# Performance work log

Hardware: AMD Instinct MI355X
Metric: run time of the kernel (lower is better)

The kernel has to match this reference:

```python
import jax, jax.numpy as jnp
import numpy as np

N, DEG, FIN, HID, OUT = 50000, 16, 128, 128, 64


def setup_inputs() -> dict:
    key = jax.random.key(0)
    ks = jax.random.split(key, 32)
    x = jax.random.normal(ks[0], (N, FIN), dtype=jnp.float32)
    src = jax.random.randint(ks[1], (N * DEG,), 0, N, dtype=jnp.int32)
    dst = jnp.repeat(jnp.arange(N, dtype=jnp.int32), DEG)  # sorted by target, fixed degree
    edge_index = jnp.stack([src, dst])  # [2, E]
    dims = [(FIN, HID), (HID, HID), (HID, OUT)]
    params = {}
    i = 2
    for l, (fi, fo) in enumerate(dims, 1):
        s_lstm = 1.0 / np.sqrt(fi)
        params[f"W_ih{l}"] = jax.random.normal(ks[i + 0], (4 * fi, fi)) * s_lstm
        params[f"W_hh{l}"] = jax.random.normal(ks[i + 1], (4 * fi, fi)) * s_lstm
        params[f"b_ih{l}"] = jax.random.normal(ks[i + 2], (4 * fi,)) * s_lstm
        params[f"b_hh{l}"] = jax.random.normal(ks[i + 3], (4 * fi,)) * s_lstm
        params[f"Wl{l}"] = jax.random.normal(ks[i + 4], (fo, fi)) * (1.0 / np.sqrt(fi))
        params[f"bl{l}"] = jnp.zeros((fo,), jnp.float32)
        params[f"Wr{l}"] = jax.random.normal(ks[i + 5], (fo, fi)) * (1.0 / np.sqrt(fi))
        i += 6
    return {"x": x, "edge_index": edge_index, **params}


def _lstm_last(neigh, Wih, Whh, bih, bhh):
    # neigh: [N, deg, Fi]; PyTorch LSTM gate order i,f,g,o; return last-step output h.
    h0 = jnp.zeros((neigh.shape[0], Wih.shape[0] // 4), neigh.dtype)
    bias = bih + bhh

    def step(carry, xt):
        h, c = carry
        g = xt @ Wih.T + h @ Whh.T + bias
        i, f, gg, o = jnp.split(g, 4, axis=-1)
        c = jax.nn.sigmoid(f) * c + jax.nn.sigmoid(i) * jnp.tanh(gg)
        h = jax.nn.sigmoid(o) * jnp.tanh(c)
        return (h, c), None

    (h, _), _ = jax.lax.scan(step, (h0, h0), jnp.swapaxes(neigh, 0, 1))
    return h


def _sage_layer(x, src2d, Wih, Whh, bih, bhh, Wl, bl, Wr):
    neigh = x[src2d]  # gather: [N, deg, Fi]
    aggr = _lstm_last(neigh, Wih, Whh, bih, bhh)  # [N, Fi]
    return aggr @ Wl.T + bl + x @ Wr.T  # lin_l(aggr) + lin_r(x)


def reference(x, edge_index,
              W_ih1, W_hh1, b_ih1, b_hh1, Wl1, bl1, Wr1,
              W_ih2, W_hh2, b_ih2, b_hh2, Wl2, bl2, Wr2,
              W_ih3, W_hh3, b_ih3, b_hh3, Wl3, bl3, Wr3):
    n = x.shape[0]
    src2d = edge_index[0].reshape(n, -1)  # fixed-degree, dst-sorted edge list
    h = _sage_layer(x, src2d, W_ih1, W_hh1, b_ih1, b_hh1, Wl1, bl1, Wr1)
    h = jax.nn.relu(h)  # dropout is identity in eval mode
    h = _sage_layer(h, src2d, W_ih2, W_hh2, b_ih2, b_hh2, Wl2, bl2, Wr2)
    h = jax.nn.relu(h)
    return _sage_layer(h, src2d, W_ih3, W_hh3, b_ih3, b_hh3, Wl3, bl3, Wr3)
```

## Files before the change

### kernel.cpp

```cpp
#include <hip/hip_runtime.h>
#include <cstddef>
#include <cstdint>

typedef __attribute__((ext_vector_type(4))) float f32x4;
typedef __attribute__((ext_vector_type(8))) short short8;

#define HID 128
#define NK1 -1.4426950408889634f
#define PK2 2.8853900817779268f

#define BAR_LGKM() __asm__ volatile("s_waitcnt lgkmcnt(0)\ns_barrier" ::: "memory")
#define STEP_BAR() __asm__ volatile("s_waitcnt vmcnt(0) lgkmcnt(0)\ns_barrier" ::: "memory")

__device__ __forceinline__ short f2bf(float f) {
  unsigned u = __builtin_bit_cast(unsigned, f);
  u += 0x7FFFu + ((u >> 16) & 1u);
  return (short)(u >> 16);
}
__device__ __forceinline__ unsigned pack_bf2(float a, float b) {
  unsigned ua = __builtin_bit_cast(unsigned, a) + 0x8000u;
  unsigned ub = __builtin_bit_cast(unsigned, b) + 0x8000u;
  return __builtin_amdgcn_perm(ub, ua, 0x07060302u);
}
__device__ __forceinline__ float2 unpack2v(int w) {
  float2 r;
  r.x = __builtin_bit_cast(float, (unsigned)(w << 16));
  r.y = __builtin_bit_cast(float, (unsigned)w & 0xffff0000u);
  return r;
}

__device__ __forceinline__ float lstm_elem(float si, float sf, float sg, float so, float& c) {
  float Ei = __builtin_amdgcn_exp2f(si);
  float Ef = __builtin_amdgcn_exp2f(sf);
  float Tg = __builtin_amdgcn_exp2f(sg);
  float Eo = __builtin_amdgcn_exp2f(so);
  float u = 1.0f + Ei, w = 1.0f + Ef, v = Tg + 1.0f, Tm = Tg - 1.0f;
  float t0 = u * v;
  float num = __builtin_fmaf(c, t0, w * Tm);
  float cn = num * __builtin_amdgcn_rcpf(w * t0);
  c = cn;
  float Tc = __builtin_amdgcn_exp2f(PK2 * cn);
  return (Tc - 1.0f) * __builtin_amdgcn_rcpf((1.0f + Eo) * (Tc + 1.0f));
}

__global__ void conv_x_kernel(const float* __restrict__ x, short* __restrict__ xb, int n) {
  int i = blockIdx.x * blockDim.x + threadIdx.x;
  int stride = gridDim.x * blockDim.x;
  for (; i < n; i += stride) xb[i] = f2bf(x[i]);
}

__global__ void conv_layer_kernel(const float* __restrict__ Wih, const float* __restrict__ Whh,
                                  const float* __restrict__ bih, const float* __restrict__ bhh,
                                  const float* __restrict__ Wl, const float* __restrict__ Wr, int foK,
                                  short* __restrict__ wihB, short* __restrict__ whhB,
                                  short* __restrict__ wlB, short* __restrict__ wrB,
                                  float* __restrict__ bsum) {
  int i = blockIdx.x * blockDim.x + threadIdx.x;
  if (i < 512 * HID) {
    float sc = ((i >> 14) == 2) ? PK2 : NK1;
    wihB[i] = f2bf(Wih[i] * sc);
    whhB[i] = f2bf(Whh[i] * sc);
  }
  if (i < foK) { wlB[i] = f2bf(Wl[i]); wrB[i] = f2bf(Wr[i]); }
  if (i < 512) bsum[i] = (bih[i] + bhh[i]) * (((i >> 7) == 2) ? PK2 : NK1);
}

#define OSTR 524
__global__ __launch_bounds__(512, 4) void pgemm_kernel(
    const short* __restrict__ A, const short* __restrict__ W,
    const float* __restrict__ bias, short* __restrict__ out, int M, int ntiles) {
  __shared__ short ldsO[32 * OSTR];
  const int tid = threadIdx.x;
  const int wave = tid >> 6, lane = tid & 63;
  const int quad = lane >> 4, nn = lane & 15;
  const int cbase = wave * 64;

  short8 wreg[4][4];
#pragma unroll
  for (int kt = 0; kt < 4; ++kt)
#pragma unroll
    for (int nt = 0; nt < 4; ++nt)
      wreg[kt][nt] = *(const short8*)(W + (size_t)(cbase + nt * 16 + nn) * HID + kt * 32 + quad * 8);
  f32x4 bias4[4];
#pragma unroll
  for (int nt = 0; nt < 4; ++nt)
#pragma unroll
    for (int r = 0; r < 4; ++r) bias4[nt][r] = bias[cbase + nt * 16 + quad * 4 + r];

#pragma unroll 1
  for (int rt = blockIdx.x; rt < ntiles; rt += gridDim.x) {
    const int row0 = rt * 32;
    f32x4 acc[2][4];
#pragma unroll
    for (int b = 0; b < 2; ++b)
#pragma unroll
      for (int nt = 0; nt < 4; ++nt) acc[b][nt] = bias4[nt];
#pragma unroll
    for (int kt = 0; kt < 4; ++kt) {
      int r0 = row0 + nn;      if (r0 > M - 1) r0 = M - 1;
      int r1 = row0 + 16 + nn; if (r1 > M - 1) r1 = M - 1;
      short8 af0 = *(const short8*)(A + (size_t)r0 * HID + kt * 32 + quad * 8);
      short8 af1 = *(const short8*)(A + (size_t)r1 * HID + kt * 32 + quad * 8);
#pragma unroll
      for (int nt = 0; nt < 4; ++nt) {
        acc[0][nt] = __builtin_amdgcn_mfma_f32_16x16x32_bf16(wreg[kt][nt], af0, acc[0][nt], 0, 0, 0);
        acc[1][nt] = __builtin_amdgcn_mfma_f32_16x16x32_bf16(wreg[kt][nt], af1, acc[1][nt], 0, 0, 0);
      }
    }
    BAR_LGKM();
#pragma unroll
    for (int b = 0; b < 2; ++b)
#pragma unroll
      for (int nt = 0; nt < 4; ++nt) {
        uint2 pk;
        pk.x = pack_bf2(acc[b][nt][0], acc[b][nt][1]);
        pk.y = pack_bf2(acc[b][nt][2], acc[b][nt][3]);
        *(uint2*)(ldsO + (b * 16 + nn) * OSTR + cbase + nt * 16 + quad * 4) = pk;
      }
    BAR_LGKM();
#pragma unroll
    for (int idx = tid; idx < 32 * 64; idx += 512) {
      int row = idx >> 6, c8 = (idx & 63) * 8;
      if (row0 + row < M)
        *(short8*)(out + (size_t)(row0 + row) * 512 + c8) = *(const short8*)(ldsO + row * OSTR + c8);
    }
  }
}

template <int FO, bool RELU, bool OUTF32>
__global__ __launch_bounds__(256, 4) void outgemm_kernel(
    const short* __restrict__ A1, const short* __restrict__ W1,
    const short* __restrict__ A2, const short* __restrict__ W2,
    const float* __restrict__ bias,
    short* __restrict__ outB, float* __restrict__ outF, int M, int ntiles) {
  const int NTW = FO / 64;
  __shared__ char osm[8704];
  short* ldsO = (short*)osm;
  float* ldsF = (float*)osm;
  const int tid = threadIdx.x;
  const int wave = tid >> 6, lane = tid & 63;
  const int quad = lane >> 4, nn = lane & 15;
  const int cbase = wave * (FO / 4);

  short8 w1r[4][NTW], w2r[4][NTW];
#pragma unroll
  for (int kt = 0; kt < 4; ++kt)
#pragma unroll
    for (int nt = 0; nt < NTW; ++nt) {
      w1r[kt][nt] = *(const short8*)(W1 + (size_t)(cbase + nt * 16 + nn) * HID + kt * 32 + quad * 8);
      w2r[kt][nt] = *(const short8*)(W2 + (size_t)(cbase + nt * 16 + nn) * HID + kt * 32 + quad * 8);
    }
  f32x4 bias4[NTW];
#pragma unroll
  for (int nt = 0; nt < NTW; ++nt)
#pragma unroll
    for (int r = 0; r < 4; ++r) bias4[nt][r] = bias[cbase + nt * 16 + quad * 4 + r];

#pragma unroll 1
  for (int rt = blockIdx.x; rt < ntiles; rt += gridDim.x) {
    const int row0 = rt * 32;
    f32x4 acc[2][NTW];
#pragma unroll
    for (int b = 0; b < 2; ++b)
#pragma unroll
      for (int nt = 0; nt < NTW; ++nt) acc[b][nt] = bias4[nt];

#pragma unroll
    for (int kt = 0; kt < 4; ++kt) {
      int r0 = row0 + nn;      if (r0 > M - 1) r0 = M - 1;
      int r1 = row0 + 16 + nn; if (r1 > M - 1) r1 = M - 1;
      short8 a10 = *(const short8*)(A1 + (size_t)r0 * HID + kt * 32 + quad * 8);
      short8 a11 = *(const short8*)(A1 + (size_t)r1 * HID + kt * 32 + quad * 8);
      short8 a20 = *(const short8*)(A2 + (size_t)r0 * HID + kt * 32 + quad * 8);
      short8 a21 = *(const short8*)(A2 + (size_t)r1 * HID + kt * 32 + quad * 8);
#pragma unroll
      for (int nt = 0; nt < NTW; ++nt) {
        acc[0][nt] = __builtin_amdgcn_mfma_f32_16x16x32_bf16(w1r[kt][nt], a10, acc[0][nt], 0, 0, 0);
        acc[1][nt] = __builtin_amdgcn_mfma_f32_16x16x32_bf16(w1r[kt][nt], a11, acc[1][nt], 0, 0, 0);
        acc[0][nt] = __builtin_amdgcn_mfma_f32_16x16x32_bf16(w2r[kt][nt], a20, acc[0][nt], 0, 0, 0);
        acc[1][nt] = __builtin_amdgcn_mfma_f32_16x16x32_bf16(w2r[kt][nt], a21, acc[1][nt], 0, 0, 0);
      }
    }
    BAR_LGKM();
#pragma unroll
    for (int b = 0; b < 2; ++b)
#pragma unroll
      for (int nt = 0; nt < NTW; ++nt) {
        f32x4 v = acc[b][nt];
        if (RELU) {
#pragma unroll
          for (int r = 0; r < 4; ++r) v[r] = fmaxf(v[r], 0.0f);
        }
        int lrow = b * 16 + nn;
        if (OUTF32) {
          *(f32x4*)(ldsF + lrow * 68 + cbase + nt * 16 + quad * 4) = v;
        } else {
          uint2 pk;
          pk.x = pack_bf2(v[0], v[1]);
          pk.y = pack_bf2(v[2], v[3]);
          *(uint2*)(ldsO + lrow * 136 + cbase + nt * 16 + quad * 4) = pk;
        }
      }
    BAR_LGKM();
    if (OUTF32) {
#pragma unroll
      for (int idx = tid; idx < 32 * 16; idx += 256) {
        int row = idx >> 4, c4 = (idx & 15) * 4;
        if (row0 + row < M)
          *(f32x4*)(outF + (size_t)(row0 + row) * 64 + c4) = *(const f32x4*)(ldsF + row * 68 + c4);
      }
    } else {
#pragma unroll
      for (int idx = tid; idx < 32 * 16; idx += 256) {
        int row = idx >> 4, c8 = (idx & 15) * 8;
        if (row0 + row < M)
          *(short8*)(outB + (size_t)(row0 + row) * 128 + c8) = *(const short8*)(ldsO + row * 136 + c8);
      }
    }
  }
}

#define NPB 16
#define PSTR 520
#define HSTR 152
#define LSTM_LDS_BYTES ((2 * NPB * PSTR + 2 * NPB * HSTR) * 2 + 256 * 4)

__global__ __launch_bounds__(512, 4) void lstm_steps_kernel(
    const short* __restrict__ P, const short* __restrict__ Whh,
    const int* __restrict__ src, short* __restrict__ aggr, int M, int ntiles) {
  extern __shared__ char smem[];
  short* Pb = (short*)smem;
  short* Hb = Pb + 2 * NPB * PSTR;
  int* srcL = (int*)(Hb + 2 * NPB * HSTR);

  const int tid = threadIdx.x;
  const int wave = tid >> 6, lane = tid & 63;
  const int quad = lane >> 4, nn = lane & 15;
  const int r0row = wave * 2, r1row = wave * 2 + 1;

  short8 wreg[4][4];
#pragma unroll
  for (int kt = 0; kt < 4; ++kt)
#pragma unroll
    for (int q = 0; q < 4; ++q)
      wreg[kt][q] = *(const short8*)(Whh + (size_t)(q * 128 + wave * 16 + nn) * HID + kt * 32 + quad * 8);

#pragma unroll 1
  for (int tile = blockIdx.x; tile < ntiles; tile += gridDim.x) {
    const int nodeBase = tile * NPB;
    if (tid < 256) {
      int node = nodeBase + (tid >> 4);
      srcL[tid] = (node < M) ? src[nodeBase * 16 + tid] : 0;
    }
    float c_st[4] = {0.f, 0.f, 0.f, 0.f};
    BAR_LGKM();

    int sA = srcL[r0row * 16 + 0], sB = srcL[r1row * 16 + 0];
    __builtin_amdgcn_global_load_lds(
        (const __attribute__((address_space(1))) unsigned int*)(P + (size_t)sA * 512 + lane * 8),
        (__attribute__((address_space(3))) unsigned int*)(Pb + r0row * PSTR), 16, 0, 0);
    __builtin_amdgcn_global_load_lds(
        (const __attribute__((address_space(1))) unsigned int*)(P + (size_t)sB * 512 + lane * 8),
        (__attribute__((address_space(3))) unsigned int*)(Pb + r1row * PSTR), 16, 0, 0);
    sA = srcL[r0row * 16 + 1];
    sB = srcL[r1row * 16 + 1];

#pragma unroll 1
    for (int t = 0; t < 16; ++t) {
      short* Pc = Pb + (t & 1) * NPB * PSTR;
      short* Pn = Pb + ((t + 1) & 1) * NPB * PSTR;
      const short* Hp = Hb + ((t + 1) & 1) * NPB * HSTR;
      short* Hw = Hb + (t & 1) * NPB * HSTR;

      STEP_BAR();

      const short* pR = Pc + nn * PSTR + wave * 16 + quad * 4;
      uint2 p0 = *(const uint2*)(pR + 0 * 128);
      uint2 p1 = *(const uint2*)(pR + 1 * 128);
      uint2 p2 = *(const uint2*)(pR + 2 * 128);
      uint2 p3 = *(const uint2*)(pR + 3 * 128);
      f32x4 acc[4];
      {
        float2 a0 = unpack2v(p0.x), a1 = unpack2v(p0.y);
        acc[0][0] = a0.x; acc[0][1] = a0.y; acc[0][2] = a1.x; acc[0][3] = a1.y;
        float2 b0 = unpack2v(p1.x), b1 = unpack2v(p1.y);
        acc[1][0] = b0.x; acc[1][1] = b0.y; acc[1][2] = b1.x; acc[1][3] = b1.y;
        float2 c0 = unpack2v(p2.x), c1 = unpack2v(p2.y);
        acc[2][0] = c0.x; acc[2][1] = c0.y; acc[2][2] = c1.x; acc[2][3] = c1.y;
        float2 d0 = unpack2v(p3.x), d1 = unpack2v(p3.y);
        acc[3][0] = d0.x; acc[3][1] = d0.y; acc[3][2] = d1.x; acc[3][3] = d1.y;
      }

      if (t < 15) {
        __builtin_amdgcn_global_load_lds(
            (const __attribute__((address_space(1))) unsigned int*)(P + (size_t)sA * 512 + lane * 8),
            (__attribute__((address_space(3))) unsigned int*)(Pn + r0row * PSTR), 16, 0, 0);
        __builtin_amdgcn_global_load_lds(
            (const __attribute__((address_space(1))) unsigned int*)(P + (size_t)sB * 512 + lane * 8),
            (__attribute__((address_space(3))) unsigned int*)(Pn + r1row * PSTR), 16, 0, 0);
        int tn = (t + 2 < 16) ? t + 2 : 15;
        sA = srcL[r0row * 16 + tn];
        sB = srcL[r1row * 16 + tn];
      }

      if (t) {
#pragma unroll
        for (int kt = 0; kt < 4; ++kt) {
          short8 hb = *(const short8*)(Hp + nn * HSTR + kt * 32 + quad * 8);
#pragma unroll
          for (int q = 0; q < 4; ++q)
            acc[q] = __builtin_amdgcn_mfma_f32_16x16x32_bf16(wreg[kt][q], hb, acc[q], 0, 0, 0);
        }
      }

      float hv[4];
#pragma unroll
      for (int r = 0; r < 4; ++r)
        hv[r] = lstm_elem(acc[0][r], acc[1][r], acc[2][r], acc[3][r], c_st[r]);
      uint2 pk;
      pk.x = pack_bf2(hv[0], hv[1]);
      pk.y = pack_bf2(hv[2], hv[3]);
      *(uint2*)(Hw + nn * HSTR + wave * 16 + quad * 4) = pk;
    }

    BAR_LGKM();
    if (tid < 256) {
      int rrow = tid >> 4, off = (tid & 15) * 8;
      int node = nodeBase + rrow;
      if (node < M)
        *(short8*)(aggr + (size_t)node * HID + off) = *(const short8*)(Hb + NPB * HSTR + rrow * HSTR + off);
    }
  }
}

extern "C" void kernel_launch(void* const* d_in, const int* in_sizes, int n_in,
                              void* d_out, int out_size, void* d_ws, size_t ws_size,
                              hipStream_t stream) {
  const float* x = (const float*)d_in[0];
  const int* src = (const int*)d_in[1];
  const float* Wih[3] = {(const float*)d_in[2], (const float*)d_in[9], (const float*)d_in[16]};
  const float* Whh[3] = {(const float*)d_in[3], (const float*)d_in[10], (const float*)d_in[17]};
  const float* bih[3] = {(const float*)d_in[4], (const float*)d_in[11], (const float*)d_in[18]};
  const float* bhh[3] = {(const float*)d_in[5], (const float*)d_in[12], (const float*)d_in[19]};
  const float* Wl[3]  = {(const float*)d_in[6], (const float*)d_in[13], (const float*)d_in[20]};
  const float* bl[3]  = {(const float*)d_in[7], (const float*)d_in[14], (const float*)d_in[21]};
  const float* Wr[3]  = {(const float*)d_in[8], (const float*)d_in[15], (const float*)d_in[22]};

  const int M = in_sizes[0] / HID;

  char* ws = (char*)d_ws;
  size_t off = 0;
  auto alloc = [&](size_t bytes) -> void* {
    void* p = ws + off;
    off += (bytes + 255) & ~(size_t)255;
    return p;
  };
  short* curA = (short*)alloc((size_t)M * HID * 2);
  short* curB = (short*)alloc((size_t)M * HID * 2);
  short* aggr = (short*)alloc((size_t)M * HID * 2);
  short* Pbuf = (short*)alloc((size_t)M * 512 * 2);
  short* wihB[3]; short* whhB[3]; short* wlB[3]; short* wrB[3]; float* bsum[3];
  for (int l = 0; l < 3; ++l) {
    wihB[l] = (short*)alloc(512 * HID * 2);
    whhB[l] = (short*)alloc(512 * HID * 2);
    wlB[l]  = (short*)alloc(HID * HID * 2);
    wrB[l]  = (short*)alloc(HID * HID * 2);
    bsum[l] = (float*)alloc(512 * 4);
  }

  const int nltiles = (M + NPB - 1) / NPB;
  const int ntiles = (M + 31) / 32;

  (void)hipFuncSetAttribute((const void*)lstm_steps_kernel,
                            hipFuncAttributeMaxDynamicSharedMemorySize, LSTM_LDS_BYTES);

  conv_x_kernel<<<2048, 256, 0, stream>>>(x, curA, M * HID);
  for (int l = 0; l < 3; ++l) {
    const int Fo = (l == 2) ? 64 : 128;
    conv_layer_kernel<<<256, 256, 0, stream>>>(Wih[l], Whh[l], bih[l], bhh[l], Wl[l], Wr[l],
                                               Fo * HID, wihB[l], whhB[l], wlB[l], wrB[l], bsum[l]);
  }

  short* cur = curA;
  short* nxt = curB;
  for (int l = 0; l < 3; ++l) {
    pgemm_kernel<<<784, 512, 0, stream>>>(cur, wihB[l], bsum[l], Pbuf, M, ntiles);
    lstm_steps_kernel<<<768, 512, LSTM_LDS_BYTES, stream>>>(Pbuf, whhB[l], src, aggr, M, nltiles);
    if (l < 2) {
      outgemm_kernel<128, true, false><<<784, 256, 0, stream>>>(
          aggr, wlB[l], cur, wrB[l], bl[l], nxt, nullptr, M, ntiles);
      short* tswap = cur; cur = nxt; nxt = tswap;
    } else {
      outgemm_kernel<64, false, true><<<784, 256, 0, stream>>>(
          aggr, wlB[l], cur, wrB[l], bl[l], nullptr, (float*)d_out, M, ntiles);
    }
  }
}
```

Baseline: 811.9 us.

## Triple-buffer gathered P rows in LSTM step kernel with two-step prefetch

The LSTM recurrence kernel now keeps three LDS buffers for the gathered input-projection rows instead of two, and issues loads two timesteps ahead. The per-step barrier waits with vmcnt(2) instead of vmcnt(0), so one step's gather can stay in flight while the current step computes. This hides more random-gather latency behind the serial MFMA/gate work, at the cost of more LDS per block (possibly lower occupancy). Grid size drops from 768 to 512 blocks. Loads are now issued every step, including redundant ones at the tail.

```diff
diff --git a/kernel.cpp b/kernel.cpp
--- a/kernel.cpp
+++ b/kernel.cpp
@@ -10,7 +10,7 @@
 #define PK2 2.8853900817779268f
 
 #define BAR_LGKM() __asm__ volatile("s_waitcnt lgkmcnt(0)\ns_barrier" ::: "memory")
-#define STEP_BAR() __asm__ volatile("s_waitcnt vmcnt(0) lgkmcnt(0)\ns_barrier" ::: "memory")
+#define STEP_BAR2() __asm__ volatile("s_waitcnt vmcnt(2) lgkmcnt(0)\ns_barrier" ::: "memory")
 
 __device__ __forceinline__ short f2bf(float f) {
   unsigned u = __builtin_bit_cast(unsigned, f);
@@ -223,14 +223,14 @@
 #define NPB 16
 #define PSTR 520
 #define HSTR 152
-#define LSTM_LDS_BYTES ((2 * NPB * PSTR + 2 * NPB * HSTR) * 2 + 256 * 4)
+#define LSTM_LDS_BYTES ((3 * NPB * PSTR + 2 * NPB * HSTR) * 2 + 256 * 4)
 
 __global__ __launch_bounds__(512, 4) void lstm_steps_kernel(
     const short* __restrict__ P, const short* __restrict__ Whh,
     const int* __restrict__ src, short* __restrict__ aggr, int M, int ntiles) {
   extern __shared__ char smem[];
   short* Pb = (short*)smem;
-  short* Hb = Pb + 2 * NPB * PSTR;
+  short* Hb = Pb + 3 * NPB * PSTR;
   int* srcL = (int*)(Hb + 2 * NPB * HSTR);
 
   const int tid = threadIdx.x;
@@ -255,24 +255,35 @@
     float c_st[4] = {0.f, 0.f, 0.f, 0.f};
     BAR_LGKM();
 
-    int sA = srcL[r0row * 16 + 0], sB = srcL[r1row * 16 + 0];
-    __builtin_amdgcn_global_load_lds(
-        (const __attribute__((address_space(1))) unsigned int*)(P + (size_t)sA * 512 + lane * 8),
-        (__attribute__((address_space(3))) unsigned int*)(Pb + r0row * PSTR), 16, 0, 0);
-    __builtin_amdgcn_global_load_lds(
-        (const __attribute__((address_space(1))) unsigned int*)(P + (size_t)sB * 512 + lane * 8),
-        (__attribute__((address_space(3))) unsigned int*)(Pb + r1row * PSTR), 16, 0, 0);
-    sA = srcL[r0row * 16 + 1];
-    sB = srcL[r1row * 16 + 1];
-
+    {
+      int s0A = srcL[r0row * 16 + 0], s0B = srcL[r1row * 16 + 0];
+      __builtin_amdgcn_global_load_lds(
+          (const __attribute__((address_space(1))) unsigned int*)(P + (size_t)s0A * 512 + lane * 8),
+          (__attribute__((address_space(3))) unsigned int*)(Pb + r0row * PSTR), 16, 0, 0);
+      __builtin_amdgcn_global_load_lds(
+          (const __attribute__((address_space(1))) unsigned int*)(P + (size_t)s0B * 512 + lane * 8),
+          (__attribute__((address_space(3))) unsigned int*)(Pb + r1row * PSTR), 16, 0, 0);
+      int s1A = srcL[r0row * 16 + 1], s1B = srcL[r1row * 16 + 1];
+      __builtin_amdgcn_global_load_lds(
+          (const __attribute__((address_space(1))) unsigned int*)(P + (size_t)s1A * 512 + lane * 8),
+          (__attribute__((address_space(3))) unsigned int*)(Pb + NPB * PSTR + r0row * PSTR), 16, 0, 0);
+      __builtin_amdgcn_global_load_lds(
+          (const __attribute__((address_space(1))) unsigned int*)(P + (size_t)s1B * 512 + lane * 8),
+          (__attribute__((address_space(3))) unsigned int*)(Pb + NPB * PSTR + r1row * PSTR), 16, 0, 0);
+    }
+    int sA = srcL[r0row * 16 + 2], sB = srcL[r1row * 16 + 2];
+
+    int pc = 0, pg = 2;
 #pragma unroll 1
     for (int t = 0; t < 16; ++t) {
-      short* Pc = Pb + (t & 1) * NPB * PSTR;
-      short* Pn = Pb + ((t + 1) & 1) * NPB * PSTR;
+      short* Pc = Pb + pc * NPB * PSTR;
+      short* Pg = Pb + pg * NPB * PSTR;
       const short* Hp = Hb + ((t + 1) & 1) * NPB * HSTR;
       short* Hw = Hb + (t & 1) * NPB * HSTR;
-
-      STEP_BAR();
+      pc = (pc == 2) ? 0 : pc + 1;
+      pg = (pg == 2) ? 0 : pg + 1;
+
+      STEP_BAR2();
 
       const short* pR = Pc + nn * PSTR + wave * 16 + quad * 4;
       uint2 p0 = *(const uint2*)(pR + 0 * 128);
@@ -291,14 +302,14 @@
         acc[3][0] = d0.x; acc[3][1] = d0.y; acc[3][2] = d1.x; acc[3][3] = d1.y;
       }
 
-      if (t < 15) {
-        __builtin_amdgcn_global_load_lds(
-            (const __attribute__((address_space(1))) unsigned int*)(P + (size_t)sA * 512 + lane * 8),
-            (__attribute__((address_space(3))) unsigned int*)(Pn + r0row * PSTR), 16, 0, 0);
-        __builtin_amdgcn_global_load_lds(
-            (const __attribute__((address_space(1))) unsigned int*)(P + (size_t)sB * 512 + lane * 8),
-            (__attribute__((address_space(3))) unsigned int*)(Pn + r1row * PSTR), 16, 0, 0);
-        int tn = (t + 2 < 16) ? t + 2 : 15;
+      __builtin_amdgcn_global_load_lds(
+          (const __attribute__((address_space(1))) unsigned int*)(P + (size_t)sA * 512 + lane * 8),
+          (__attribute__((address_space(3))) unsigned int*)(Pg + r0row * PSTR), 16, 0, 0);
+      __builtin_amdgcn_global_load_lds(
+          (const __attribute__((address_space(1))) unsigned int*)(P + (size_t)sB * 512 + lane * 8),
+          (__attribute__((address_space(3))) unsigned int*)(Pg + r1row * PSTR), 16, 0, 0);
+      {
+        int tn = (t + 3 < 16) ? t + 3 : 15;
         sA = srcL[r0row * 16 + tn];
         sB = srcL[r1row * 16 + tn];
       }
@@ -385,7 +396,7 @@
   short* nxt = curB;
   for (int l = 0; l < 3; ++l) {
     pgemm_kernel<<<784, 512, 0, stream>>>(cur, wihB[l], bsum[l], Pbuf, M, ntiles);
-    lstm_steps_kernel<<<768, 512, LSTM_LDS_BYTES, stream>>>(Pbuf, whhB[l], src, aggr, M, nltiles);
+    lstm_steps_kernel<<<512, 512, LSTM_LDS_BYTES, stream>>>(Pbuf, whhB[l], src, aggr, M, nltiles);
     if (l < 2) {
       outgemm_kernel<128, true, false><<<784, 256, 0, stream>>>(
           aggr, wlB[l], cur, wrB[l], bl[l], nxt, nullptr, M, ntiles);
```

Result: faster. 787.4 us (-3.0%).
